# Optimization experiments

Measured on AMD Instinct MI355X. Metric: run time of the kernel, lower is better.

Reference implementation:

```python
import jax, jax.numpy as jnp
import numpy as np

SEQ, HID = 4096, 1024
NEG_INF = -10000000000.0


def setup_inputs() -> dict:
    key = jax.random.key(0)
    ks = jax.random.split(key, 6)
    s = 1.0 / np.sqrt(HID)
    return {
        "query": jax.random.normal(ks[0], (SEQ, HID), jnp.float32),
        "key": jax.random.normal(ks[1], (SEQ, HID), jnp.float32),
        "value": jax.random.normal(ks[2], (SEQ, HID), jnp.float32),
        # SASRec causal mask: allowed positions are 1, masked are 0
        "mask": jnp.tril(jnp.ones((SEQ, SEQ), jnp.int32)),
        "Wq": jax.random.normal(ks[3], (HID, HID), jnp.float32) * s,
        "Wk": jax.random.normal(ks[4], (HID, HID), jnp.float32) * s,
        "Wv": jax.random.normal(ks[5], (HID, HID), jnp.float32) * s,
    }


def reference(query, key, value, mask, Wq, Wk, Wv):
    # nn.Linear(bias=False): y = x @ W.T
    Q = query @ Wq.T   # [S, H]
    K = key @ Wk.T     # [S, H]
    V = value @ Wv.T   # [S, H]
    scale = jnp.sqrt(jnp.asarray(HID, Q.dtype))
    energy = (Q @ K.T) / scale                      # [S, S]
    energy = jnp.where(mask == 0, NEG_INF, energy)  # masked_fill
    attention = jax.nn.softmax(energy, axis=-1)     # [S, S]
    x = attention @ V                               # dropout is identity in eval
    return (x, attention)
```

## Files before the change

### kernel.cpp

```cpp
#include <hip/hip_runtime.h>

#define SEQ 4096
#define HID 1024

typedef _Float16 f16x4 __attribute__((ext_vector_type(4)));
typedef _Float16 f16x8 __attribute__((ext_vector_type(8)));
typedef float    f32x4 __attribute__((ext_vector_type(4)));

__device__ __forceinline__ void gld16(const void* g, void* l) {
    __builtin_amdgcn_global_load_lds(
        (const __attribute__((address_space(1))) unsigned int*)g,
        (__attribute__((address_space(3))) unsigned int*)l, 16, 0, 0);
}

__global__ __launch_bounds__(256) void cast_all(
    const float4* __restrict__ q, const float4* __restrict__ k,
    const float4* __restrict__ v,
    const float4* __restrict__ wq, const float4* __restrict__ wk,
    const float4* __restrict__ wv,
    f16x4* __restrict__ qh, f16x4* __restrict__ kh, f16x4* __restrict__ vh,
    f16x4* __restrict__ wqh, f16x4* __restrict__ wkh, f16x4* __restrict__ wvh,
    int nX4, int nW4) {
    int t = blockIdx.x * 256 + threadIdx.x;
    const float4 *a, *b, *c; f16x4 *da, *db, *dc; int idx;
    if (t < nX4) { a = q; b = k; c = v; da = qh; db = kh; dc = vh; idx = t; }
    else if (t < nX4 + nW4) {
        idx = t - nX4;
        a = wq; b = wk; c = wv; da = wqh; db = wkh; dc = wvh;
    } else return;
    float4 va = a[idx], vb = b[idx], vc = c[idx];
    f16x4 oa = {(_Float16)va.x, (_Float16)va.y, (_Float16)va.z, (_Float16)va.w};
    f16x4 ob = {(_Float16)vb.x, (_Float16)vb.y, (_Float16)vb.z, (_Float16)vb.w};
    f16x4 oc = {(_Float16)vc.x, (_Float16)vc.y, (_Float16)vc.z, (_Float16)vc.w};
    da[idx] = oa; db[idx] = ob; dc[idx] = oc;
}

__global__ __launch_bounds__(256) void transpose_f16(
    const _Float16* __restrict__ src, _Float16* __restrict__ dst,
    int R, int C) {
    __shared__ _Float16 tile[32][33];
    int c0 = blockIdx.x * 32, r0 = blockIdx.y * 32;
    int tr = threadIdx.x >> 5, tc = threadIdx.x & 31;
#pragma unroll
    for (int q = 0; q < 4; ++q)
        tile[tr + q * 8][tc] = src[(size_t)(r0 + tr + q * 8) * C + c0 + tc];
    __syncthreads();
#pragma unroll
    for (int q = 0; q < 4; ++q)
        dst[(size_t)(c0 + tr + q * 8) * R + r0 + tc] = tile[tc][tr + q * 8];
}

template <typename OutT, bool TRI_SKIP, bool TRI_K, int ZMODE>
__global__ __launch_bounds__(256) void gemm_nt(
    const _Float16* __restrict__ A, const _Float16* __restrict__ Bt,
    OutT* __restrict__ C, int M, int N, int K, float scale,
    long sA, long sB, long sC, int KC, float* __restrict__ PB,
    const _Float16* __restrict__ A2, const _Float16* __restrict__ B2,
    OutT* __restrict__ C2, int N2) {
    __shared__ __attribute__((aligned(16))) _Float16 As[2 * 128 * 32];
    __shared__ __attribute__((aligned(16))) _Float16 Bs[2 * 128 * 32];

    int bm = blockIdx.y;
    int bn = blockIdx.x;
    if (TRI_SKIP && bn > bm) return;
    const _Float16* Ap = A;
    const _Float16* Bp = Bt;
    OutT* Cp = C;
    int Nloc = N;
    if (ZMODE == 6 && blockIdx.y >= 32) {
        const int lin = (blockIdx.y - 32) * 8 + blockIdx.x;
        bm = lin >> 5; bn = lin & 31;
        Ap = A2; Bp = B2; Cp = C2; Nloc = N2;
    }

    int kstart = 0, kend, zslot = -1;
    if (ZMODE == 4) {
        const int y = 79 - (int)blockIdx.y;
        int g = 0;
        while (4 * (g + 1) * (g + 2) <= y) ++g;
        const int rem = y - 4 * g * (g + 1);
        const int m   = g + 1;
        const int rg  = rem / m;
        bm = 8 * g + rg;
        const int z = rem - rg * m;
        kstart = z * KC;
        kend   = min((bm + 1) * 128, kstart + KC);
        if (z > 0) zslot = 4 * g * (g - 1) + rg * g + (z - 1);
    } else if (ZMODE == 5) {
        kstart = blockIdx.z * KC;
        kend   = kstart + KC;
        Cp += (long)blockIdx.z * sC;
    } else {
        kend = TRI_K ? min(K, (bm + 1) * 128) : K;
    }

    const int tid = threadIdx.x;
    const int tr  = tid >> 2;
    const int tc8 = (tid & 3) * 8;

    const _Float16* Ab = Ap + (size_t)bm * 128 * K;
    const _Float16* Bb = Bp + (size_t)bn * 128 * K;

    const int wave = tid >> 6;
    const int lane = tid & 63;
    const int wm = (wave >> 1) * 64;
    const int wn = (wave & 1) * 64;
    const int lr = lane & 15;
    const int lk = (lane >> 4) * 8;

    f32x4 acc[4][4];
#pragma unroll
    for (int i = 0; i < 4; ++i)
#pragma unroll
        for (int j = 0; j < 4; ++j) acc[i][j] = (f32x4)0.0f;

    for (int k0 = kstart; k0 < kend; k0 += 64) {
#pragma unroll
        for (int h = 0; h < 2; ++h) {
            const int kk = k0 + h * 32, off = h * 4096;
            gld16(Ab + (size_t)tr * K        + kk + tc8, &As[off + tr * 32 + tc8]);
            gld16(Ab + (size_t)(64 + tr) * K + kk + tc8, &As[off + (64 + tr) * 32 + tc8]);
            gld16(Bb + (size_t)tr * K        + kk + tc8, &Bs[off + tr * 32 + tc8]);
            gld16(Bb + (size_t)(64 + tr) * K + kk + tc8, &Bs[off + (64 + tr) * 32 + tc8]);
        }
        __syncthreads();

#pragma unroll
        for (int h = 0; h < 2; ++h) {
            const int off = h * 4096;
            f16x8 af[4], bfr[4];
#pragma unroll
            for (int i = 0; i < 4; ++i)
                af[i] = *(const f16x8*)&As[off + (wm + i * 16 + lr) * 32 + lk];
#pragma unroll
            for (int j = 0; j < 4; ++j)
                bfr[j] = *(const f16x8*)&Bs[off + (wn + j * 16 + lr) * 32 + lk];
#pragma unroll
            for (int i = 0; i < 4; ++i)
#pragma unroll
                for (int j = 0; j < 4; ++j)
                    acc[i][j] = __builtin_amdgcn_mfma_f32_16x16x32_f16(
                        af[i], bfr[j], acc[i][j], 0, 0, 0);
        }
        __syncthreads();
    }

    const int er = (lane >> 4) * 4;
    const int ec = lane & 15;
#pragma unroll
    for (int i = 0; i < 4; ++i) {
#pragma unroll
        for (int j = 0; j < 4; ++j) {
            const int lrow0 = wm + i * 16 + er;
            const int col   = bn * 128 + wn + j * 16 + ec;
#pragma unroll
            for (int r = 0; r < 4; ++r) {
                const float val = acc[i][j][r] * scale;
                if (ZMODE == 4 && zslot >= 0)
                    PB[(size_t)(zslot * 128 + lrow0 + r) * 1024 + col] = val;
                else
                    Cp[(long)(bm * 128 + lrow0 + r) * Nloc + col] = (OutT)val;
            }
        }
    }
}

__global__ __launch_bounds__(256) void reduce_pv(
    float* __restrict__ out, const float* __restrict__ PB) {
    const int row = 1024 + blockIdx.x;
    const int bm  = row >> 7;
    const int g   = bm >> 3;
    const int slot0 = 4 * g * (g - 1) + (bm - 8 * g) * g;
    const int rloc  = row & 127;
    float4* o = (float4*)(out + (size_t)row * 1024) + threadIdx.x;
    float4 acc = *o;
    for (int z = 0; z < g; ++z) {
        const float4 p = *((const float4*)(PB +
            ((size_t)(slot0 + z) * 128 + rloc) * 1024) + threadIdx.x);
        acc.x += p.x; acc.y += p.y; acc.z += p.z; acc.w += p.w;
    }
    *o = acc;
}

__global__ __launch_bounds__(256) void softmax_causal(
    _Float16* __restrict__ EP0, const _Float16* __restrict__ EP1,
    float* __restrict__ att, int S) {
    __shared__ float rowbuf[SEQ];
    __shared__ float red[8];
    const int i   = blockIdx.x;
    const int tid = threadIdx.x;
    const int wv  = tid >> 6, ln = tid & 63;
    _Float16* E0row = EP0 + (size_t)i * S;
    const _Float16* E1row = EP1 + (size_t)i * S;

    float lmax = -INFINITY;
    for (int j8 = tid * 8; j8 <= i; j8 += 2048) {
        f16x8 a8 = *(const f16x8*)&E0row[j8];
        f16x8 b8 = *(const f16x8*)&E1row[j8];
#pragma unroll
        for (int u = 0; u < 8; ++u) {
            int j = j8 + u;
            if (j <= i) {
                float vv = (float)a8[u] + (float)b8[u];
                rowbuf[j] = vv;
                lmax = fmaxf(lmax, vv);
            }
        }
    }
#pragma unroll
    for (int o = 32; o > 0; o >>= 1) lmax = fmaxf(lmax, __shfl_down(lmax, o, 64));
    if (ln == 0) red[wv] = lmax;
    __syncthreads();
    if (tid == 0)
        red[4] = fmaxf(fmaxf(red[0], red[1]), fmaxf(red[2], red[3]));
    __syncthreads();
    const float rmax = red[4];

    float lsum = 0.0f;
    for (int j4 = tid * 4; j4 <= i; j4 += 1024) {
        float4 e = *(float4*)&rowbuf[j4];
        float4 o;
        o.x = (j4     <= i) ? __expf(e.x - rmax) : 0.f;
        o.y = (j4 + 1 <= i) ? __expf(e.y - rmax) : 0.f;
        o.z = (j4 + 2 <= i) ? __expf(e.z - rmax) : 0.f;
        o.w = (j4 + 3 <= i) ? __expf(e.w - rmax) : 0.f;
        *(float4*)&rowbuf[j4] = o;
        lsum += o.x + o.y + o.z + o.w;
    }
#pragma unroll
    for (int o = 32; o > 0; o >>= 1) lsum += __shfl_down(lsum, o, 64);
    __syncthreads();
    if (ln == 0) red[wv] = lsum;
    __syncthreads();
    if (tid == 0)
        red[4] = red[0] + red[1] + red[2] + red[3];
    __syncthreads();
    const float rinv = 1.0f / red[4];

    float* arow = att + (size_t)i * S;
    const int jlim = ((i >> 7) + 1) << 7;
    for (int j4 = tid * 4; j4 < S; j4 += 1024) {
        float4 a;
        a.x = (j4     <= i) ? rowbuf[j4]     * rinv : 0.f;
        a.y = (j4 + 1 <= i) ? rowbuf[j4 + 1] * rinv : 0.f;
        a.z = (j4 + 2 <= i) ? rowbuf[j4 + 2] * rinv : 0.f;
        a.w = (j4 + 3 <= i) ? rowbuf[j4 + 3] * rinv : 0.f;
        *(float4*)&arow[j4] = a;
        if (j4 < jlim) {
            f16x4 p = {(_Float16)a.x, (_Float16)a.y, (_Float16)a.z, (_Float16)a.w};
            *(f16x4*)&E0row[j4] = p;
        }
    }
}

extern "C" void kernel_launch(void* const* d_in, const int* in_sizes, int n_in,
                              void* d_out, int out_size, void* d_ws, size_t ws_size,
                              hipStream_t stream) {
    const float* q  = (const float*)d_in[0];
    const float* k  = (const float*)d_in[1];
    const float* v  = (const float*)d_in[2];
    const float* Wq = (const float*)d_in[4];
    const float* Wk = (const float*)d_in[5];
    const float* Wv = (const float*)d_in[6];

    float* out_x   = (float*)d_out;
    float* out_att = out_x + (size_t)SEQ * HID;

    char* ws = (char*)d_ws;
    const size_t SH = (size_t)SEQ * HID * sizeof(_Float16);
    const size_t HH = (size_t)HID * HID * sizeof(_Float16);
    _Float16* qh  = (_Float16*)(ws);
    _Float16* vh  = (_Float16*)(ws + SH);
    _Float16* wqh = (_Float16*)(ws + 2 * SH);
    _Float16* wkh = (_Float16*)(ws + 2 * SH + HH);
    _Float16* wvh = (_Float16*)(ws + 2 * SH + 2 * HH);
    _Float16* WqT = (_Float16*)(ws + 2 * SH + 3 * HH);
    _Float16* WkT = (_Float16*)(ws + 2 * SH + 4 * HH);
    _Float16* Mt  = (_Float16*)(ws + 2 * SH + 5 * HH);
    _Float16* EP1 = (_Float16*)(ws);
    _Float16* kh  = (_Float16*)(ws + 4 * SH);
    _Float16* Qh  = (_Float16*)(ws + 5 * SH);
    _Float16* VT  = (_Float16*)(ws + 6 * SH);
    _Float16* EP0 = (_Float16*)(ws + 7 * SH);
    float* Pbuf = (float*)ws;

    const int nX4 = SEQ * HID / 4, nW4 = HID * HID / 4;
    cast_all<<<(nX4 + nW4 + 255) / 256, 256, 0, stream>>>(
        (const float4*)q, (const float4*)k, (const float4*)v,
        (const float4*)Wq, (const float4*)Wk, (const float4*)Wv,
        (f16x4*)qh, (f16x4*)kh, (f16x4*)vh,
        (f16x4*)wqh, (f16x4*)wkh, (f16x4*)wvh, nX4, nW4);

    transpose_f16<<<dim3(HID / 32, HID / 32), 256, 0, stream>>>(wqh, WqT, HID, HID);
    transpose_f16<<<dim3(HID / 32, HID / 32), 256, 0, stream>>>(wkh, WkT, HID, HID);
    gemm_nt<_Float16, false, false, 0><<<dim3(HID / 128, HID / 128), 256, 0, stream>>>(
        WkT, WqT, Mt, HID, HID, HID, 1.0f, 0, 0, 0, 0, nullptr,
        nullptr, nullptr, nullptr, 0);

    gemm_nt<_Float16, false, false, 6><<<dim3(8, 64), 256, 0, stream>>>(
        qh, Mt, Qh, SEQ, HID, HID, 1.0f, 0, 0, 0, 0, nullptr,
        wvh, vh, VT, SEQ);

    gemm_nt<_Float16, true, false, 5><<<dim3(SEQ / 128, SEQ / 128, 2), 256, 0, stream>>>(
        Qh, kh, EP0, SEQ, SEQ, HID, 0.03125f,
        0, 0, (long)(EP1 - EP0), 512, nullptr, nullptr, nullptr, nullptr, 0);

    softmax_causal<<<SEQ, 256, 0, stream>>>(EP0, EP1, out_att, SEQ);

    gemm_nt<float, false, true, 4><<<dim3(HID / 128, 80), 256, 0, stream>>>(
        EP0, VT, out_x, SEQ, HID, SEQ, 1.0f, 0, 0, 0, 1024, Pbuf,
        nullptr, nullptr, nullptr, 0);

    reduce_pv<<<3072, 256, 0, stream>>>(out_x, Pbuf);
}
```

Measured before the change: 318.2 us.

## Project Q and K directly instead of folding Wk^T·Wq into a fused matrix

Drops the two weight transposes and the Wk^T·Wq product that built a combined matrix M, so Q is no longer computed as q·M with K left as the raw cast input. Q, K and V^T are now computed directly in one batched launch with three z-slices (Q and K via strides, V^T via the second operand set). This removes two transpose launches and one dependent GEMM from the critical path. In exchange it adds a full K projection (SEQ×HID×HID) on top of the V^T and Q projections, so projection FLOPs grow by roughly half.

Result: faster. 306.9 us (-3.6%).

```diff
diff --git a/kernel.cpp b/kernel.cpp
--- a/kernel.cpp
+++ b/kernel.cpp
@@ -35,21 +35,6 @@
     da[idx] = oa; db[idx] = ob; dc[idx] = oc;
 }
 
-__global__ __launch_bounds__(256) void transpose_f16(
-    const _Float16* __restrict__ src, _Float16* __restrict__ dst,
-    int R, int C) {
-    __shared__ _Float16 tile[32][33];
-    int c0 = blockIdx.x * 32, r0 = blockIdx.y * 32;
-    int tr = threadIdx.x >> 5, tc = threadIdx.x & 31;
-#pragma unroll
-    for (int q = 0; q < 4; ++q)
-        tile[tr + q * 8][tc] = src[(size_t)(r0 + tr + q * 8) * C + c0 + tc];
-    __syncthreads();
-#pragma unroll
-    for (int q = 0; q < 4; ++q)
-        dst[(size_t)(c0 + tr + q * 8) * R + r0 + tc] = tile[tc][tr + q * 8];
-}
-
 template <typename OutT, bool TRI_SKIP, bool TRI_K, int ZMODE>
 __global__ __launch_bounds__(256) void gemm_nt(
     const _Float16* __restrict__ A, const _Float16* __restrict__ Bt,
@@ -67,10 +52,15 @@
     const _Float16* Bp = Bt;
     OutT* Cp = C;
     int Nloc = N;
-    if (ZMODE == 6 && blockIdx.y >= 32) {
-        const int lin = (blockIdx.y - 32) * 8 + blockIdx.x;
-        bm = lin >> 5; bn = lin & 31;
-        Ap = A2; Bp = B2; Cp = C2; Nloc = N2;
+    if (ZMODE == 7) {
+        if (blockIdx.z < 2) {
+            Ap = A  + (long)blockIdx.z * sA;
+            Bp = Bt + (long)blockIdx.z * sB;
+            Cp = C  + (long)blockIdx.z * sC;
+        } else {
+            Ap = A2; Bp = B2; Cp = C2; Nloc = N2;
+            bm = blockIdx.x; bn = blockIdx.y;
+        }
     }
 
     int kstart = 0, kend, zslot = -1;
@@ -274,14 +264,12 @@
     _Float16* wqh = (_Float16*)(ws + 2 * SH);
     _Float16* wkh = (_Float16*)(ws + 2 * SH + HH);
     _Float16* wvh = (_Float16*)(ws + 2 * SH + 2 * HH);
-    _Float16* WqT = (_Float16*)(ws + 2 * SH + 3 * HH);
-    _Float16* WkT = (_Float16*)(ws + 2 * SH + 4 * HH);
-    _Float16* Mt  = (_Float16*)(ws + 2 * SH + 5 * HH);
     _Float16* EP1 = (_Float16*)(ws);
     _Float16* kh  = (_Float16*)(ws + 4 * SH);
     _Float16* Qh  = (_Float16*)(ws + 5 * SH);
-    _Float16* VT  = (_Float16*)(ws + 6 * SH);
-    _Float16* EP0 = (_Float16*)(ws + 7 * SH);
+    _Float16* Kh  = (_Float16*)(ws + 6 * SH);
+    _Float16* VT  = (_Float16*)(ws + 7 * SH);
+    _Float16* EP0 = (_Float16*)(ws + 8 * SH);
     float* Pbuf = (float*)ws;
 
     const int nX4 = SEQ * HID / 4, nW4 = HID * HID / 4;
@@ -291,18 +279,13 @@
         (f16x4*)qh, (f16x4*)kh, (f16x4*)vh,
         (f16x4*)wqh, (f16x4*)wkh, (f16x4*)wvh, nX4, nW4);
 
-    transpose_f16<<<dim3(HID / 32, HID / 32), 256, 0, stream>>>(wqh, WqT, HID, HID);
-    transpose_f16<<<dim3(HID / 32, HID / 32), 256, 0, stream>>>(wkh, WkT, HID, HID);
-    gemm_nt<_Float16, false, false, 0><<<dim3(HID / 128, HID / 128), 256, 0, stream>>>(
-        WkT, WqT, Mt, HID, HID, HID, 1.0f, 0, 0, 0, 0, nullptr,
-        nullptr, nullptr, nullptr, 0);
-
-    gemm_nt<_Float16, false, false, 6><<<dim3(8, 64), 256, 0, stream>>>(
-        qh, Mt, Qh, SEQ, HID, HID, 1.0f, 0, 0, 0, 0, nullptr,
+    gemm_nt<_Float16, false, false, 7><<<dim3(HID / 128, SEQ / 128, 3), 256, 0, stream>>>(
+        qh, wqh, Qh, SEQ, HID, HID, 1.0f,
+        (long)(kh - qh), (long)(wkh - wqh), (long)(Kh - Qh), 0, nullptr,
         wvh, vh, VT, SEQ);
 
     gemm_nt<_Float16, true, false, 5><<<dim3(SEQ / 128, SEQ / 128, 2), 256, 0, stream>>>(
-        Qh, kh, EP0, SEQ, SEQ, HID, 0.03125f,
+        Qh, Kh, EP0, SEQ, SEQ, HID, 0.03125f,
         0, 0, (long)(EP1 - EP0), 512, nullptr, nullptr, nullptr, nullptr, 0);
 
     softmax_causal<<<SEQ, 256, 0, stream>>>(EP0, EP1, out_att, SEQ);
```
